# Kernel tuning notes

Hardware: AMD Instinct MI355X
Metric: run time of the kernel (lower is better)

The kernel has to match this reference:

```python
import jax, jax.numpy as jnp
import numpy as np

N0, N1, N2 = 200000, 50000, 10000
E0, E1 = 800000, 160000
IN_DIM, H1, H2, EMB = 256, 256, 256, 128


def gcn_layer(h_src, src_idx, dst_idx, n_src, n_dst, W, b):
    # DGL GraphConv, norm='both': D_dst^{-1/2} A D_src^{-1/2} X W + b,
    # degrees clamped to min 1 (allow_zero_in_degree=True -> zero rows stay zero).
    ones = jnp.ones(src_idx.shape[0], dtype=h_src.dtype)
    out_deg = jnp.clip(jax.ops.segment_sum(ones, src_idx, num_segments=n_src), 1.0)
    in_deg = jnp.clip(jax.ops.segment_sum(ones, dst_idx, num_segments=n_dst), 1.0)
    # in_dim >= out_dim here, so DGL multiplies by W first then aggregates;
    # result is identical either way.
    h = (h_src * jax.lax.rsqrt(out_deg)[:, None]) @ W          # [n_src, out]
    agg = jax.ops.segment_sum(h[src_idx], dst_idx, num_segments=n_dst)  # [n_dst, out]
    return agg * jax.lax.rsqrt(in_deg)[:, None] + b


def setup_inputs() -> dict:
    key = jax.random.key(0)
    ks = jax.random.split(key, 10)
    h = jax.random.normal(ks[0], (N0, IN_DIM), dtype=jnp.float32)
    src0 = jax.random.randint(ks[1], (E0,), 0, N0, dtype=jnp.int32)
    dst0 = jax.random.randint(ks[2], (E0,), 0, N1, dtype=jnp.int32)
    src1 = jax.random.randint(ks[3], (E1,), 0, N1, dtype=jnp.int32)
    dst1 = jax.random.randint(ks[4], (E1,), 0, N2, dtype=jnp.int32)
    s1 = 1.0 / np.sqrt(IN_DIM)
    s2 = 1.0 / np.sqrt(H1)
    sp = 1.0 / np.sqrt(H2)
    W1 = jax.random.normal(ks[5], (IN_DIM, H1), dtype=jnp.float32) * s1
    W2 = jax.random.normal(ks[6], (H1, H2), dtype=jnp.float32) * s2
    Wp = jax.random.normal(ks[7], (H2, EMB), dtype=jnp.float32) * sp
    b1 = jnp.zeros((H1,), dtype=jnp.float32)
    b2 = jnp.zeros((H2,), dtype=jnp.float32)
    bp = jnp.zeros((EMB,), dtype=jnp.float32)
    return {"h": h, "src0": src0, "dst0": dst0, "src1": src1, "dst1": dst1,
            "W1": W1, "b1": b1, "W2": W2, "b2": b2, "Wp": Wp, "bp": bp}


def reference(h, src0, dst0, src1, dst1, W1, b1, W2, b2, Wp, bp):
    h = gcn_layer(h, src0, dst0, N0, N1, W1, b1)   # [N1, H1]
    h = gcn_layer(h, src1, dst1, N1, N2, W2, b2)   # [N2, H2]
    return h @ Wp + bp                             # [N2, EMB]
```

## Files before the change

kernel.cpp:

```cpp
#include <hip/hip_runtime.h>
#include <cstddef>

#define N0 200000
#define N1 50000
#define N2 10000
#define E0 800000
#define E1 160000

typedef short bf16x8 __attribute__((ext_vector_type(8)));
typedef float f32x4 __attribute__((ext_vector_type(4)));

__device__ __forceinline__ unsigned short f2bf(float f) {
    unsigned int u = __float_as_uint(f);
    unsigned int r = (u + 0x7FFF + ((u >> 16) & 1)) >> 16;
    return (unsigned short)r;
}

__global__ void count_kernel(const int* __restrict__ src, const int* __restrict__ dst,
                             int* __restrict__ out_cnt, int* __restrict__ in_cnt,
                             int* __restrict__ rank, int E) {
    int e = blockIdx.x * 256 + threadIdx.x;
    if (e < E) {
        atomicAdd(&out_cnt[src[e]], 1);
        rank[e] = atomicAdd(&in_cnt[dst[e]], 1);
    }
}

__global__ void scales_kernel(const int* __restrict__ cnt, float* __restrict__ rs, int n) {
    int i = blockIdx.x * 256 + threadIdx.x;
    if (i < n) rs[i] = rsqrtf((float)max(cnt[i], 1));
}

__global__ __launch_bounds__(1024) void scan_kernel(const int* __restrict__ cnt,
                                                    int* __restrict__ rowptr, int n) {
    __shared__ int partial[1024];
    const int t = threadIdx.x;
    const int chunk = (n + 1023) / 1024;
    const int begin = t * chunk;
    const int end = min(begin + chunk, n);
    int sum = 0;
    for (int i = begin; i < end; i++) sum += cnt[i];
    partial[t] = sum;
    __syncthreads();
    for (int off = 1; off < 1024; off <<= 1) {
        int v = (t >= off) ? partial[t - off] : 0;
        __syncthreads();
        partial[t] += v;
        __syncthreads();
    }
    int run = partial[t] - sum;
    for (int i = begin; i < end; i++) {
        rowptr[i] = run;
        run += cnt[i];
    }
    if (t == 1023) rowptr[n] = partial[1023];
}

__global__ void fill_kernel(const int* __restrict__ src, const int* __restrict__ dst,
                            const int* __restrict__ rank, const int* __restrict__ rowptr,
                            int* __restrict__ csr, int E) {
    int e = blockIdx.x * 256 + threadIdx.x;
    if (e < E) csr[rowptr[dst[e]] + rank[e]] = src[e];
}

__global__ __launch_bounds__(256) void gather_kernel(const float* __restrict__ hsrc,
                                                     const float* __restrict__ rs_src,
                                                     const float* __restrict__ rs_dst,
                                                     const int* __restrict__ rowptr,
                                                     const int* __restrict__ csr,
                                                     float* __restrict__ agg, int n_dst) {
    int w    = (blockIdx.x * 256 + threadIdx.x) >> 6;
    int lane = threadIdx.x & 63;
    if (w >= n_dst) return;
    int e   = rowptr[w];
    int end = rowptr[w + 1];
    float4 acc = make_float4(0.f, 0.f, 0.f, 0.f);
    for (; e + 3 < end; e += 4) {
        int s0 = csr[e], s1 = csr[e + 1], s2 = csr[e + 2], s3 = csr[e + 3];
        float sc0 = rs_src[s0], sc1 = rs_src[s1], sc2 = rs_src[s2], sc3 = rs_src[s3];
        float4 v0 = ((const float4*)(hsrc + (size_t)s0 * 256))[lane];
        float4 v1 = ((const float4*)(hsrc + (size_t)s1 * 256))[lane];
        float4 v2 = ((const float4*)(hsrc + (size_t)s2 * 256))[lane];
        float4 v3 = ((const float4*)(hsrc + (size_t)s3 * 256))[lane];
        acc.x += v0.x * sc0; acc.y += v0.y * sc0; acc.z += v0.z * sc0; acc.w += v0.w * sc0;
        acc.x += v1.x * sc1; acc.y += v1.y * sc1; acc.z += v1.z * sc1; acc.w += v1.w * sc1;
        acc.x += v2.x * sc2; acc.y += v2.y * sc2; acc.z += v2.z * sc2; acc.w += v2.w * sc2;
        acc.x += v3.x * sc3; acc.y += v3.y * sc3; acc.z += v3.z * sc3; acc.w += v3.w * sc3;
    }
    for (; e < end; e++) {
        int s0 = csr[e];
        float sc0 = rs_src[s0];
        float4 v0 = ((const float4*)(hsrc + (size_t)s0 * 256))[lane];
        acc.x += v0.x * sc0; acc.y += v0.y * sc0; acc.z += v0.z * sc0; acc.w += v0.w * sc0;
    }
    float sd = rs_dst[w];
    acc.x *= sd; acc.y *= sd; acc.z *= sd; acc.w *= sd;
    ((float4*)(agg + (size_t)w * 256))[lane] = acc;
}

__global__ void pack_b_kernel(const float* __restrict__ W, unsigned short* __restrict__ Bp,
                              int K, int N) {
    int tid = blockIdx.x * 256 + threadIdx.x;
    int total = (N / 16) * (K / 32) * 64;
    if (tid >= total) return;
    int lane = tid & 63;
    int rest = tid >> 6;
    int s  = rest % (K / 32);
    int ct = rest / (K / 32);
    int col = ct * 16 + (lane & 15);
    int k0  = s * 32 + (lane >> 4) * 8;
    unsigned short* dst = Bp + (size_t)tid * 8;
#pragma unroll
    for (int j = 0; j < 8; j++) dst[j] = f2bf(W[(size_t)(k0 + j) * N + col]);
}

template <int NCT>
__global__ __launch_bounds__(256) void gemm_mfma(const float* __restrict__ A,
                                                 const unsigned short* __restrict__ Bp,
                                                 const float* __restrict__ bias,
                                                 float* __restrict__ C, int M, int N) {
    const int lane = threadIdx.x & 63;
    const int wave = threadIdx.x >> 6;
    const int rowBase = blockIdx.x * 64;
    const int colBase = wave * (NCT * 16);
    const int lm = lane & 15;
    const int quad = lane >> 4;

    f32x4 acc[4][NCT];
#pragma unroll
    for (int rt = 0; rt < 4; rt++)
#pragma unroll
        for (int ct = 0; ct < NCT; ct++) acc[rt][ct] = (f32x4){0.f, 0.f, 0.f, 0.f};

    const float* ap[4];
#pragma unroll
    for (int rt = 0; rt < 4; rt++) {
        int r = min(rowBase + rt * 16 + lm, M - 1);
        ap[rt] = A + (size_t)r * 256 + quad * 8;
    }

#pragma unroll
    for (int s = 0; s < 8; s++) {
        bf16x8 afrag[4];
#pragma unroll
        for (int rt = 0; rt < 4; rt++) {
            const float* p = ap[rt] + s * 32;
            float4 x = *(const float4*)p;
            float4 y = *(const float4*)(p + 4);
            union { unsigned short u[8]; bf16x8 v; } af;
            af.u[0] = f2bf(x.x); af.u[1] = f2bf(x.y); af.u[2] = f2bf(x.z); af.u[3] = f2bf(x.w);
            af.u[4] = f2bf(y.x); af.u[5] = f2bf(y.y); af.u[6] = f2bf(y.z); af.u[7] = f2bf(y.w);
            afrag[rt] = af.v;
        }
#pragma unroll
        for (int ct = 0; ct < NCT; ct++) {
            bf16x8 bfrag = *(const bf16x8*)(Bp + (((size_t)(wave * NCT + ct) * 8 + s) * 64 + lane) * 8);
#pragma unroll
            for (int rt = 0; rt < 4; rt++)
                acc[rt][ct] = __builtin_amdgcn_mfma_f32_16x16x32_bf16(afrag[rt], bfrag, acc[rt][ct], 0, 0, 0);
        }
    }

#pragma unroll
    for (int ct = 0; ct < NCT; ct++) {
        float bv = bias[colBase + ct * 16 + lm];
#pragma unroll
        for (int rt = 0; rt < 4; rt++) {
#pragma unroll
            for (int i = 0; i < 4; i++) {
                int row = rowBase + rt * 16 + quad * 4 + i;
                if (row < M) C[(size_t)row * N + colBase + ct * 16 + lm] = acc[rt][ct][i] + bv;
            }
        }
    }
}

extern "C" void kernel_launch(void* const* d_in, const int* in_sizes, int n_in,
                              void* d_out, int out_size, void* d_ws, size_t ws_size,
                              hipStream_t stream) {
    const float* h    = (const float*)d_in[0];
    const int*   src0 = (const int*)d_in[1];
    const int*   dst0 = (const int*)d_in[2];
    const int*   src1 = (const int*)d_in[3];
    const int*   dst1 = (const int*)d_in[4];
    const float* W1   = (const float*)d_in[5];
    const float* b1   = (const float*)d_in[6];
    const float* W2   = (const float*)d_in[7];
    const float* b2   = (const float*)d_in[8];
    const float* Wp   = (const float*)d_in[9];
    const float* bp   = (const float*)d_in[10];
    float* out = (float*)d_out;

    int* ib = (int*)d_ws;
    int* cnt_out0 = ib;
    int* cnt_in0  = cnt_out0 + N0;
    int* cnt_out1 = cnt_in0 + N1;
    int* cnt_in1  = cnt_out1 + N1;
    int* rank0    = cnt_in1 + N2;
    int* rank1    = rank0 + E0;
    int* rowptr0  = rank1 + E1;
    int* rowptr1  = rowptr0 + (N1 + 1);
    int* csr0     = rowptr1 + (N2 + 1);
    int* csr1     = csr0 + E0;
    float* fb = (float*)(ib + 2290004);
    float* rs_out0 = fb;
    float* rs_in0  = rs_out0 + N0;
    float* rs_out1 = rs_in0 + N1;
    float* rs_in1  = rs_out1 + N1;
    float* h1      = rs_in1 + N2;
    float* regA    = h1 + (size_t)N1 * 256;
    float* agg0    = regA;
    float* agg1    = regA;
    float* h2      = regA + 3200000;
    unsigned short* W1p = (unsigned short*)(regA + (size_t)N1 * 256);
    unsigned short* W2p = W1p + 256 * 256;
    unsigned short* Wpp = W2p + 256 * 256;

    const int n_cnt = N0 + N1 + N1 + N2;

    hipMemsetAsync(cnt_out0, 0, (size_t)n_cnt * sizeof(int), stream);

    pack_b_kernel<<<(16 * 8 * 64 + 255) / 256, 256, 0, stream>>>(W1, W1p, 256, 256);
    pack_b_kernel<<<(16 * 8 * 64 + 255) / 256, 256, 0, stream>>>(W2, W2p, 256, 256);
    pack_b_kernel<<<(8 * 8 * 64 + 255) / 256, 256, 0, stream>>>(Wp, Wpp, 256, 128);

    count_kernel<<<(E0 + 255) / 256, 256, 0, stream>>>(src0, dst0, cnt_out0, cnt_in0, rank0, E0);
    count_kernel<<<(E1 + 255) / 256, 256, 0, stream>>>(src1, dst1, cnt_out1, cnt_in1, rank1, E1);

    scales_kernel<<<(n_cnt + 255) / 256, 256, 0, stream>>>(cnt_out0, rs_out0, n_cnt);

    scan_kernel<<<1, 1024, 0, stream>>>(cnt_in0, rowptr0, N1);
    scan_kernel<<<1, 1024, 0, stream>>>(cnt_in1, rowptr1, N2);

    fill_kernel<<<(E0 + 255) / 256, 256, 0, stream>>>(src0, dst0, rank0, rowptr0, csr0, E0);
    fill_kernel<<<(E1 + 255) / 256, 256, 0, stream>>>(src1, dst1, rank1, rowptr1, csr1, E1);

    gather_kernel<<<(N1 + 3) / 4, 256, 0, stream>>>(h, rs_out0, rs_in0, rowptr0, csr0, agg0, N1);

    gemm_mfma<4><<<(N1 + 63) / 64, 256, 0, stream>>>(agg0, W1p, b1, h1, N1, 256);

    gather_kernel<<<(N2 + 3) / 4, 256, 0, stream>>>(h1, rs_out1, rs_in1, rowptr1, csr1, agg1, N2);

    gemm_mfma<4><<<(N2 + 63) / 64, 256, 0, stream>>>(agg1, W2p, b2, h2, N2, 256);

    gemm_mfma<2><<<(N2 + 63) / 64, 256, 0, stream>>>(h2, Wpp, bp, out, N2, 128);
}
```

Measured before the change: 711.6 us.

## Transform-then-aggregate with bf16 intermediates and fuse per-graph setup kernels

Switches each GCN layer from aggregate-then-GEMM to GEMM-then-aggregate. The first layer's GEMM now runs over all 200k source rows with the out-degree scale folded into the epilogue, and its output is stored in bf16. The gather then reads half-width bf16 rows and applies the in-degree scale and bias, and all intermediate activations stay in bf16. Paired count, fill, scan and pack launches are merged into single launches. The cost is a 4x larger first GEMM (200k rows instead of 50k) traded against cheaper gathers over the 800k edges, plus extra bf16 rounding of the intermediates.

After: 730.4 us. 2.6% more time.

```diff
diff --git a/kernel.cpp b/kernel.cpp
--- a/kernel.cpp
+++ b/kernel.cpp
@@ -9,20 +9,51 @@
 
 typedef short bf16x8 __attribute__((ext_vector_type(8)));
 typedef float f32x4 __attribute__((ext_vector_type(4)));
+typedef unsigned short us4 __attribute__((ext_vector_type(4)));
 
 __device__ __forceinline__ unsigned short f2bf(float f) {
     unsigned int u = __float_as_uint(f);
     unsigned int r = (u + 0x7FFF + ((u >> 16) & 1)) >> 16;
     return (unsigned short)r;
 }
-
-__global__ void count_kernel(const int* __restrict__ src, const int* __restrict__ dst,
-                             int* __restrict__ out_cnt, int* __restrict__ in_cnt,
-                             int* __restrict__ rank, int E) {
+__device__ __forceinline__ float bf2f(unsigned short s) {
+    return __uint_as_float(((unsigned int)s) << 16);
+}
+
+__global__ void pack_all(const float* __restrict__ W1, const float* __restrict__ W2,
+                         const float* __restrict__ Wp,
+                         unsigned short* __restrict__ W1p, unsigned short* __restrict__ W2p,
+                         unsigned short* __restrict__ Wpp) {
+    int tid = blockIdx.x * 256 + threadIdx.x;
+    if (tid >= 320 * 64) return;
+    int lane = tid & 63;
+    int tile = tid >> 6;
+    const float* W; unsigned short* Bp; int N; int lt;
+    if (tile < 128)      { W = W1; Bp = W1p; N = 256; lt = tile; }
+    else if (tile < 256) { W = W2; Bp = W2p; N = 256; lt = tile - 128; }
+    else                 { W = Wp; Bp = Wpp; N = 128; lt = tile - 256; }
+    int s  = lt & 7;
+    int ct = lt >> 3;
+    int col = ct * 16 + (lane & 15);
+    int k0  = s * 32 + (lane >> 4) * 8;
+    unsigned short* dst = Bp + ((size_t)lt * 64 + lane) * 8;
+#pragma unroll
+    for (int j = 0; j < 8; j++) dst[j] = f2bf(W[(size_t)(k0 + j) * N + col]);
+}
+
+__global__ void count_all(const int* __restrict__ src0, const int* __restrict__ dst0,
+                          const int* __restrict__ src1, const int* __restrict__ dst1,
+                          int* __restrict__ cnt_out0, int* __restrict__ cnt_in0,
+                          int* __restrict__ cnt_out1, int* __restrict__ cnt_in1,
+                          int* __restrict__ rank0, int* __restrict__ rank1) {
     int e = blockIdx.x * 256 + threadIdx.x;
-    if (e < E) {
-        atomicAdd(&out_cnt[src[e]], 1);
-        rank[e] = atomicAdd(&in_cnt[dst[e]], 1);
+    if (e < E0) {
+        atomicAdd(&cnt_out0[src0[e]], 1);
+        rank0[e] = atomicAdd(&cnt_in0[dst0[e]], 1);
+    } else if (e < E0 + E1) {
+        int f = e - E0;
+        atomicAdd(&cnt_out1[src1[f]], 1);
+        rank1[f] = atomicAdd(&cnt_in1[dst1[f]], 1);
     }
 }
 
@@ -31,8 +62,11 @@
     if (i < n) rs[i] = rsqrtf((float)max(cnt[i], 1));
 }
 
-__global__ __launch_bounds__(1024) void scan_kernel(const int* __restrict__ cnt,
-                                                    int* __restrict__ rowptr, int n) {
+__global__ __launch_bounds__(1024) void scan2(const int* __restrict__ cnt_in0, int* __restrict__ rowptr0,
+                                              const int* __restrict__ cnt_in1, int* __restrict__ rowptr1) {
+    const int* cnt = blockIdx.x ? cnt_in1 : cnt_in0;
+    int* rowptr    = blockIdx.x ? rowptr1 : rowptr0;
+    const int n    = blockIdx.x ? N2 : N1;
     __shared__ int partial[1024];
     const int t = threadIdx.x;
     const int chunk = (n + 1023) / 1024;
@@ -56,69 +90,26 @@
     if (t == 1023) rowptr[n] = partial[1023];
 }
 
-__global__ void fill_kernel(const int* __restrict__ src, const int* __restrict__ dst,
-                            const int* __restrict__ rank, const int* __restrict__ rowptr,
-                            int* __restrict__ csr, int E) {
+__global__ void fill_all(const int* __restrict__ src0, const int* __restrict__ dst0,
+                         const int* __restrict__ src1, const int* __restrict__ dst1,
+                         const int* __restrict__ rank0, const int* __restrict__ rank1,
+                         const int* __restrict__ rowptr0, const int* __restrict__ rowptr1,
+                         int* __restrict__ csr0, int* __restrict__ csr1) {
     int e = blockIdx.x * 256 + threadIdx.x;
-    if (e < E) csr[rowptr[dst[e]] + rank[e]] = src[e];
-}
-
-__global__ __launch_bounds__(256) void gather_kernel(const float* __restrict__ hsrc,
-                                                     const float* __restrict__ rs_src,
-                                                     const float* __restrict__ rs_dst,
-                                                     const int* __restrict__ rowptr,
-                                                     const int* __restrict__ csr,
-                                                     float* __restrict__ agg, int n_dst) {
-    int w    = (blockIdx.x * 256 + threadIdx.x) >> 6;
-    int lane = threadIdx.x & 63;
-    if (w >= n_dst) return;
-    int e   = rowptr[w];
-    int end = rowptr[w + 1];
-    float4 acc = make_float4(0.f, 0.f, 0.f, 0.f);
-    for (; e + 3 < end; e += 4) {
-        int s0 = csr[e], s1 = csr[e + 1], s2 = csr[e + 2], s3 = csr[e + 3];
-        float sc0 = rs_src[s0], sc1 = rs_src[s1], sc2 = rs_src[s2], sc3 = rs_src[s3];
-        float4 v0 = ((const float4*)(hsrc + (size_t)s0 * 256))[lane];
-        float4 v1 = ((const float4*)(hsrc + (size_t)s1 * 256))[lane];
-        float4 v2 = ((const float4*)(hsrc + (size_t)s2 * 256))[lane];
-        float4 v3 = ((const float4*)(hsrc + (size_t)s3 * 256))[lane];
-        acc.x += v0.x * sc0; acc.y += v0.y * sc0; acc.z += v0.z * sc0; acc.w += v0.w * sc0;
-        acc.x += v1.x * sc1; acc.y += v1.y * sc1; acc.z += v1.z * sc1; acc.w += v1.w * sc1;
-        acc.x += v2.x * sc2; acc.y += v2.y * sc2; acc.z += v2.z * sc2; acc.w += v2.w * sc2;
-        acc.x += v3.x * sc3; acc.y += v3.y * sc3; acc.z += v3.z * sc3; acc.w += v3.w * sc3;
-    }
-    for (; e < end; e++) {
-        int s0 = csr[e];
-        float sc0 = rs_src[s0];
-        float4 v0 = ((const float4*)(hsrc + (size_t)s0 * 256))[lane];
-        acc.x += v0.x * sc0; acc.y += v0.y * sc0; acc.z += v0.z * sc0; acc.w += v0.w * sc0;
-    }
-    float sd = rs_dst[w];
-    acc.x *= sd; acc.y *= sd; acc.z *= sd; acc.w *= sd;
-    ((float4*)(agg + (size_t)w * 256))[lane] = acc;
-}
-
-__global__ void pack_b_kernel(const float* __restrict__ W, unsigned short* __restrict__ Bp,
-                              int K, int N) {
-    int tid = blockIdx.x * 256 + threadIdx.x;
-    int total = (N / 16) * (K / 32) * 64;
-    if (tid >= total) return;
-    int lane = tid & 63;
-    int rest = tid >> 6;
-    int s  = rest % (K / 32);
-    int ct = rest / (K / 32);
-    int col = ct * 16 + (lane & 15);
-    int k0  = s * 32 + (lane >> 4) * 8;
-    unsigned short* dst = Bp + (size_t)tid * 8;
-#pragma unroll
-    for (int j = 0; j < 8; j++) dst[j] = f2bf(W[(size_t)(k0 + j) * N + col]);
-}
-
-template <int NCT>
-__global__ __launch_bounds__(256) void gemm_mfma(const float* __restrict__ A,
+    if (e < E0) {
+        csr0[rowptr0[dst0[e]] + rank0[e]] = src0[e];
+    } else if (e < E0 + E1) {
+        int f = e - E0;
+        csr1[rowptr1[dst1[f]] + rank1[f]] = src1[f];
+    }
+}
+
+template <int NCT, bool AF32, bool OBF16>
+__global__ __launch_bounds__(256) void gemm_mfma(const void* __restrict__ A_,
                                                  const unsigned short* __restrict__ Bp,
+                                                 const float* __restrict__ rs,
                                                  const float* __restrict__ bias,
-                                                 float* __restrict__ C, int M, int N) {
+                                                 void* __restrict__ C_, int M, int N) {
     const int lane = threadIdx.x & 63;
     const int wave = threadIdx.x >> 6;
     const int rowBase = blockIdx.x * 64;
@@ -132,25 +123,29 @@
 #pragma unroll
         for (int ct = 0; ct < NCT; ct++) acc[rt][ct] = (f32x4){0.f, 0.f, 0.f, 0.f};
 
-    const float* ap[4];
-#pragma unroll
-    for (int rt = 0; rt < 4; rt++) {
-        int r = min(rowBase + rt * 16 + lm, M - 1);
-        ap[rt] = A + (size_t)r * 256 + quad * 8;
-    }
+    int rowIdx[4];
+#pragma unroll
+    for (int rt = 0; rt < 4; rt++) rowIdx[rt] = min(rowBase + rt * 16 + lm, M - 1);
+
+    const float* af32 = (const float*)A_;
+    const unsigned short* abf = (const unsigned short*)A_;
 
 #pragma unroll
     for (int s = 0; s < 8; s++) {
         bf16x8 afrag[4];
 #pragma unroll
         for (int rt = 0; rt < 4; rt++) {
-            const float* p = ap[rt] + s * 32;
-            float4 x = *(const float4*)p;
-            float4 y = *(const float4*)(p + 4);
-            union { unsigned short u[8]; bf16x8 v; } af;
-            af.u[0] = f2bf(x.x); af.u[1] = f2bf(x.y); af.u[2] = f2bf(x.z); af.u[3] = f2bf(x.w);
-            af.u[4] = f2bf(y.x); af.u[5] = f2bf(y.y); af.u[6] = f2bf(y.z); af.u[7] = f2bf(y.w);
-            afrag[rt] = af.v;
+            if (AF32) {
+                const float* p = af32 + (size_t)rowIdx[rt] * 256 + quad * 8 + s * 32;
+                float4 x = *(const float4*)p;
+                float4 y = *(const float4*)(p + 4);
+                union { unsigned short u[8]; bf16x8 v; } af;
+                af.u[0] = f2bf(x.x); af.u[1] = f2bf(x.y); af.u[2] = f2bf(x.z); af.u[3] = f2bf(x.w);
+                af.u[4] = f2bf(y.x); af.u[5] = f2bf(y.y); af.u[6] = f2bf(y.z); af.u[7] = f2bf(y.w);
+                afrag[rt] = af.v;
+            } else {
+                afrag[rt] = *(const bf16x8*)(abf + (size_t)rowIdx[rt] * 256 + quad * 8 + s * 32);
+            }
         }
 #pragma unroll
         for (int ct = 0; ct < NCT; ct++) {
@@ -162,17 +157,62 @@
     }
 
 #pragma unroll
-    for (int ct = 0; ct < NCT; ct++) {
-        float bv = bias[colBase + ct * 16 + lm];
-#pragma unroll
-        for (int rt = 0; rt < 4; rt++) {
+    for (int rt = 0; rt < 4; rt++) {
+        f32x4 rsv = (f32x4){1.f, 1.f, 1.f, 1.f};
+        if (rs) rsv = *(const f32x4*)(rs + rowBase + rt * 16 + quad * 4);
+#pragma unroll
+        for (int ct = 0; ct < NCT; ct++) {
+            int col = colBase + ct * 16 + lm;
+            float bv = bias ? bias[col] : 0.0f;
 #pragma unroll
             for (int i = 0; i < 4; i++) {
                 int row = rowBase + rt * 16 + quad * 4 + i;
-                if (row < M) C[(size_t)row * N + colBase + ct * 16 + lm] = acc[rt][ct][i] + bv;
+                if (row < M) {
+                    float v = acc[rt][ct][i] * rsv[i] + bv;
+                    if (OBF16) ((unsigned short*)C_)[(size_t)row * N + col] = f2bf(v);
+                    else       ((float*)C_)[(size_t)row * N + col] = v;
+                }
             }
         }
     }
+}
+
+__global__ __launch_bounds__(256) void gather_bf16(const unsigned short* __restrict__ Y,
+                                                   const int* __restrict__ rowptr,
+                                                   const int* __restrict__ csr,
+                                                   const float* __restrict__ rs_dst,
+                                                   const float* __restrict__ bias,
+                                                   unsigned short* __restrict__ outb, int n_dst) {
+    int w    = (blockIdx.x * 256 + threadIdx.x) >> 6;
+    int lane = threadIdx.x & 63;
+    if (w >= n_dst) return;
+    int e   = rowptr[w];
+    int end = rowptr[w + 1];
+    f32x4 acc = (f32x4){0.f, 0.f, 0.f, 0.f};
+    for (; e + 3 < end; e += 4) {
+        int s0 = csr[e], s1 = csr[e + 1], s2 = csr[e + 2], s3 = csr[e + 3];
+        us4 v0 = *(const us4*)(Y + (size_t)s0 * 256 + lane * 4);
+        us4 v1 = *(const us4*)(Y + (size_t)s1 * 256 + lane * 4);
+        us4 v2 = *(const us4*)(Y + (size_t)s2 * 256 + lane * 4);
+        us4 v3 = *(const us4*)(Y + (size_t)s3 * 256 + lane * 4);
+        acc[0] += bf2f(v0[0]) + bf2f(v1[0]) + bf2f(v2[0]) + bf2f(v3[0]);
+        acc[1] += bf2f(v0[1]) + bf2f(v1[1]) + bf2f(v2[1]) + bf2f(v3[1]);
+        acc[2] += bf2f(v0[2]) + bf2f(v1[2]) + bf2f(v2[2]) + bf2f(v3[2]);
+        acc[3] += bf2f(v0[3]) + bf2f(v1[3]) + bf2f(v2[3]) + bf2f(v3[3]);
+    }
+    for (; e < end; e++) {
+        int s0 = csr[e];
+        us4 v0 = *(const us4*)(Y + (size_t)s0 * 256 + lane * 4);
+        acc[0] += bf2f(v0[0]); acc[1] += bf2f(v0[1]); acc[2] += bf2f(v0[2]); acc[3] += bf2f(v0[3]);
+    }
+    float sd = rs_dst[w];
+    f32x4 b = *(const f32x4*)(bias + lane * 4);
+    us4 o;
+    o[0] = f2bf(acc[0] * sd + b[0]);
+    o[1] = f2bf(acc[1] * sd + b[1]);
+    o[2] = f2bf(acc[2] * sd + b[2]);
+    o[3] = f2bf(acc[3] * sd + b[3]);
+    *(us4*)(outb + (size_t)w * 256 + lane * 4) = o;
 }
 
 extern "C" void kernel_launch(void* const* d_in, const int* in_sizes, int n_in,
@@ -196,52 +236,49 @@
     int* cnt_in0  = cnt_out0 + N0;
     int* cnt_out1 = cnt_in0 + N1;
     int* cnt_in1  = cnt_out1 + N1;
-    int* rank0    = cnt_in1 + N2;
-    int* rank1    = rank0 + E0;
-    int* rowptr0  = rank1 + E1;
-    int* rowptr1  = rowptr0 + (N1 + 1);
-    int* csr0     = rowptr1 + (N2 + 1);
-    int* csr1     = csr0 + E0;
-    float* fb = (float*)(ib + 2290004);
+    int* rowptr0  = ib + 310000;
+    int* rowptr1  = ib + 360001;
+    int* csr0     = ib + 370004;
+    int* csr1     = ib + 1170004;
+    float* fb = (float*)(ib + 1330004);
     float* rs_out0 = fb;
-    float* rs_in0  = rs_out0 + N0;
-    float* rs_out1 = rs_in0 + N1;
-    float* rs_in1  = rs_out1 + N1;
-    float* h1      = rs_in1 + N2;
-    float* regA    = h1 + (size_t)N1 * 256;
-    float* agg0    = regA;
-    float* agg1    = regA;
-    float* h2      = regA + 3200000;
-    unsigned short* W1p = (unsigned short*)(regA + (size_t)N1 * 256);
-    unsigned short* W2p = W1p + 256 * 256;
-    unsigned short* Wpp = W2p + 256 * 256;
-
-    const int n_cnt = N0 + N1 + N1 + N2;
-
-    hipMemsetAsync(cnt_out0, 0, (size_t)n_cnt * sizeof(int), stream);
-
-    pack_b_kernel<<<(16 * 8 * 64 + 255) / 256, 256, 0, stream>>>(W1, W1p, 256, 256);
-    pack_b_kernel<<<(16 * 8 * 64 + 255) / 256, 256, 0, stream>>>(W2, W2p, 256, 256);
-    pack_b_kernel<<<(8 * 8 * 64 + 255) / 256, 256, 0, stream>>>(Wp, Wpp, 256, 128);
-
-    count_kernel<<<(E0 + 255) / 256, 256, 0, stream>>>(src0, dst0, cnt_out0, cnt_in0, rank0, E0);
-    count_kernel<<<(E1 + 255) / 256, 256, 0, stream>>>(src1, dst1, cnt_out1, cnt_in1, rank1, E1);
-
-    scales_kernel<<<(n_cnt + 255) / 256, 256, 0, stream>>>(cnt_out0, rs_out0, n_cnt);
-
-    scan_kernel<<<1, 1024, 0, stream>>>(cnt_in0, rowptr0, N1);
-    scan_kernel<<<1, 1024, 0, stream>>>(cnt_in1, rowptr1, N2);
-
-    fill_kernel<<<(E0 + 255) / 256, 256, 0, stream>>>(src0, dst0, rank0, rowptr0, csr0, E0);
-    fill_kernel<<<(E1 + 255) / 256, 256, 0, stream>>>(src1, dst1, rank1, rowptr1, csr1, E1);
-
-    gather_kernel<<<(N1 + 3) / 4, 256, 0, stream>>>(h, rs_out0, rs_in0, rowptr0, csr0, agg0, N1);
-
-    gemm_mfma<4><<<(N1 + 63) / 64, 256, 0, stream>>>(agg0, W1p, b1, h1, N1, 256);
-
-    gather_kernel<<<(N2 + 3) / 4, 256, 0, stream>>>(h1, rs_out1, rs_in1, rowptr1, csr1, agg1, N2);
-
-    gemm_mfma<4><<<(N2 + 63) / 64, 256, 0, stream>>>(agg1, W2p, b2, h2, N2, 256);
-
-    gemm_mfma<2><<<(N2 + 63) / 64, 256, 0, stream>>>(h2, Wpp, bp, out, N2, 128);
-}
+    float* rs_in0  = fb + 200000;
+    float* rs_out1 = fb + 250000;
+    float* rs_in1  = fb + 300000;
+    unsigned short* wpk = (unsigned short*)(fb + 310000);
+    unsigned short* W1p = wpk;
+    unsigned short* W2p = wpk + 65536;
+    unsigned short* Wpp = wpk + 131072;
+    unsigned short* R   = wpk + 163840;
+    int* rank0 = (int*)R;
+    int* rank1 = rank0 + E0;
+    unsigned short* Y1  = R;
+    unsigned short* Y2  = R;
+    unsigned short* h2b = R + (size_t)N1 * 256;
+    unsigned short* h1b = R + (size_t)N0 * 256;
+
+    hipMemsetAsync(cnt_out0, 0, (size_t)310000 * sizeof(int), stream);
+
+    pack_all<<<80, 256, 0, stream>>>(W1, W2, Wp, W1p, W2p, Wpp);
+
+    count_all<<<(E0 + E1 + 255) / 256, 256, 0, stream>>>(src0, dst0, src1, dst1,
+                                                         cnt_out0, cnt_in0, cnt_out1, cnt_in1,
+                                                         rank0, rank1);
+
+    scales_kernel<<<(310000 + 255) / 256, 256, 0, stream>>>(cnt_out0, rs_out0, 310000);
+
+    scan2<<<2, 1024, 0, stream>>>(cnt_in0, rowptr0, cnt_in1, rowptr1);
+
+    fill_all<<<(E0 + E1 + 255) / 256, 256, 0, stream>>>(src0, dst0, src1, dst1,
+                                                        rank0, rank1, rowptr0, rowptr1, csr0, csr1);
+
+    gemm_mfma<4, true, true><<<N0 / 64, 256, 0, stream>>>(h, W1p, rs_out0, nullptr, Y1, N0, 256);
+
+    gather_bf16<<<(N1 + 3) / 4, 256, 0, stream>>>(Y1, rowptr0, csr0, rs_in0, b1, h1b, N1);
+
+    gemm_mfma<4, false, true><<<(N1 + 63) / 64, 256, 0, stream>>>(h1b, W2p, rs_out1, nullptr, Y2, N1, 256);
+
+    gather_bf16<<<(N2 + 3) / 4, 256, 0, stream>>>(Y2, rowptr1, csr1, rs_in1, b2, h2b, N2);
+
+    gemm_mfma<2, false, false><<<(N2 + 63) / 64, 256, 0, stream>>>(h2b, Wpp, nullptr, bp, out, N2, 128);
+}
```
